# Kernel tuning notes

Measured on AMD Instinct MI355X. Metric: run time of the kernel, lower is better.

Reference implementation:

```python
import jax, jax.numpy as jnp
import numpy as np
import math

H, DH, DP, DE = 8, 16, 128, 32   # heads, dim_head, dim_p_embd, dim_embd
M = 64                            # number of random features
EPS = 1e-4                        # softmax_kernel eps
LN_EPS = 1e-5


def gelu(x):
    # exact tanh-approx gelu used in the source
    return 0.5 * x * (1.0 + jnp.tanh(math.sqrt(2.0 / math.pi) * (x + 0.044715 * x ** 3)))


def layernorm(x, w, b):
    mu = x.mean(-1, keepdims=True)
    var = ((x - mu) ** 2).mean(-1, keepdims=True)
    return (x - mu) / jnp.sqrt(var + LN_EPS) * w + b


def softmax_kernel(data, proj, is_query):
    # FAVOR+ positive random-feature softmax kernel
    dn = data.shape[-1] ** -0.25
    ratio = proj.shape[0] ** -0.5
    dash = jnp.einsum('bhnd,md->bhnm', dn * data, proj)
    diag = (data ** 2).sum(-1, keepdims=True) * (0.5 * dn * dn)
    unnorm = ratio * jnp.exp(dash - diag)
    if is_query:
        mx = jax.lax.stop_gradient(jnp.max(dash, axis=-1, keepdims=True))
    else:
        mx = jax.lax.stop_gradient(jnp.max(dash, axis=(-1, -2), keepdims=True))
    return unnorm * jnp.exp(-mx) + ratio * EPS, unnorm


def linear_attention(q, k, v):
    k_sum = k.sum(-2)                                        # (b,h,m)
    d_inv = 1.0 / jnp.einsum('bhnm,bhm->bhn', q, k_sum)
    ctx = jnp.einsum('bhnm,bhne->bhme', k, v)                # (b,h,m,d)
    return jnp.einsum('bhme,bhnm,bhn->bhne', ctx, q, d_inv)


def heads(t):
    b, n, _ = t.shape
    return t.reshape(b, n, H, DH).transpose(0, 2, 1, 3)      # b n (h d) -> b h n d


def setup_inputs() -> dict:
    key = jax.random.key(0)
    ks = jax.random.split(key, 12)
    B, NCTX, NQ = 16, 3200, 3072
    std = 0.02
    return {
        'x': jax.random.normal(ks[0], (B, NCTX, DE), jnp.float32),
        'y': jax.random.normal(ks[1], (2, B, NQ, DP), jnp.float32),
        'proj': jax.random.normal(ks[2], (M, DH), jnp.float32),
        'ln1_w': jnp.ones((DP,), jnp.float32), 'ln1_b': jnp.zeros((DP,), jnp.float32),
        'ln2_w': jnp.ones((DE,), jnp.float32), 'ln2_b': jnp.zeros((DE,), jnp.float32),
        'ln4_w': jnp.ones((DP,), jnp.float32), 'ln4_b': jnp.zeros((DP,), jnp.float32),
        'fc_w': std * jax.random.normal(ks[3], (DP, DP), jnp.float32),
        'fc_b': jnp.zeros((DP,), jnp.float32),
        'pr_w': std * jax.random.normal(ks[4], (DP, DP), jnp.float32),
        'pr_b': jnp.zeros((DP,), jnp.float32),
        'wq': std * jax.random.normal(ks[5], (DP, DP), jnp.float32),
        'wk': std * jax.random.normal(ks[6], (DP, DE), jnp.float32),
        'wv': std * jax.random.normal(ks[7], (DP, DE), jnp.float32),
        'wo': std * jax.random.normal(ks[8], (DP, DP), jnp.float32),
        'wo_b': jnp.zeros((DP,), jnp.float32),
    }


def reference(x, y, proj, ln1_w, ln1_b, ln2_w, ln2_b, ln4_w, ln4_b,
              fc_w, fc_b, pr_w, pr_b, wq, wk, wv, wo, wo_b):
    # --- MLP(dim_p_embd) pre-attention residual (Conv1D: x @ W + b) ---
    h = gelu(layernorm(y, ln4_w, ln4_b) @ fc_w + fc_b)
    y1 = h @ pr_w + pr_b + y                                 # (2,B,NQ,DP)

    xq = layernorm(y1, ln1_w, ln1_b)
    ctx = layernorm(x, ln2_w, ln2_b)
    B, NCTX, _ = x.shape
    NQ = y.shape[2]

    q = heads(xq.reshape(-1, NQ, DP) @ wq.T)                 # (2B,H,NQ,DH)
    k = heads(ctx @ wk.T)                                    # (B,H,NCTX,DH)
    v = heads(ctx @ wv.T)

    # temporal split: doubles the batch, drops first/last s tokens
    s = NCTX * 2 // 50
    k2 = jnp.concatenate([k[None, :, :, :-s], k[None, :, :, s:]], 0).reshape(2 * B, H, NCTX - s, DH)
    v2 = jnp.concatenate([v[None, :, :, :-s], v[None, :, :, s:]], 0).reshape(2 * B, H, NCTX - s, DH)

    qf, q_unnorm = softmax_kernel(q, proj, True)
    kf, k_unnorm = softmax_kernel(k2, proj, False)
    out = linear_attention(qf, kf, v2)                       # (2B,H,NQ,DH)

    out = out.transpose(0, 2, 1, 3).reshape(2 * B, NQ, DP) @ wo.T + wo_b
    y_out = y1 + out.reshape(y.shape)
    return y_out, q_unnorm[:, :, None], k_unnorm[:, :, None]
```

## Files before the change

### kernel.cpp

```cpp
#include <hip/hip_runtime.h>
#include <math.h>

constexpr int cH = 8;
constexpr int cDP = 128;
constexpr int cM = 64;
constexpr int cB = 16;
constexpr int cNCTX = 3200;
constexpr int cNQ = 3072;
constexpr int cSHIFT = 128;
constexpr int ROWS_Q = 2 * cB * cNQ;
constexpr int ROWS_KV = cB * cNCTX;
constexpr float cRATIO = 0.125f;
constexpr float cEPST = 0.125e-4f;
constexpr float cLNEPS = 1e-5f;

typedef float f32x4 __attribute__((ext_vector_type(4)));
typedef short short8 __attribute__((ext_vector_type(8)));
typedef _Float16 half2 __attribute__((ext_vector_type(2)));

#define MFMA16x16(a, b, c) __builtin_amdgcn_mfma_f32_16x16x32_bf16((a), (b), (c), 0, 0, 0)

__device__ __forceinline__ float wmax64(float v) {
#pragma unroll
  for (int o = 32; o; o >>= 1) v = fmaxf(v, __shfl_xor(v, o));
  return v;
}
__device__ __forceinline__ float wsum64(float v) {
#pragma unroll
  for (int o = 32; o; o >>= 1) v += __shfl_xor(v, o);
  return v;
}
__device__ __forceinline__ float gelu_f(float x) {
  return 0.5f * x * (1.0f + tanhf(0.79788456080286536f * (x + 0.044715f * x * x * x)));
}
__device__ __forceinline__ unsigned int bf16r(float f) {
  unsigned int x = __float_as_uint(f);
  return (x + 0x7fffu + ((x >> 16) & 1u)) >> 16;
}
__device__ __forceinline__ unsigned int f16r(float f) {
  _Float16 hh = (_Float16)f;
  unsigned short u;
  __builtin_memcpy(&u, &hh, 2);
  return (unsigned int)u;
}
__device__ __forceinline__ int swz(int row, int k) {
  return row * 128 + ((((k >> 3) ^ (row & 15)) << 3) | (k & 7));
}

__global__ __launch_bounds__(256) void k0_prep(
    const float* __restrict__ fcw, const float* __restrict__ prw,
    const float* __restrict__ wq, const float* __restrict__ wo,
    unsigned short* __restrict__ fcT, unsigned short* __restrict__ prT,
    unsigned short* __restrict__ wqT, unsigned short* __restrict__ woT) {
  const int mat = blockIdx.x;
  const float* src = mat == 0 ? fcw : mat == 1 ? prw : mat == 2 ? wq : wo;
  unsigned short* dst = mat == 0 ? fcT : mat == 1 ? prT : mat == 2 ? wqT : woT;
  const bool tr = (mat < 2);
  for (int i = threadIdx.x; i < 16384; i += 256) {
    int n = i >> 7, k = i & 127;
    float f = tr ? src[k * 128 + n] : src[i];
    dst[swz(n, k)] = (unsigned short)(mat == 2 ? f16r(f) : bf16r(f));
  }
}

__global__ __launch_bounds__(256, 2) void k1_mlp(
    const float* __restrict__ y,
    const float* __restrict__ ln4w, const float* __restrict__ ln4b,
    const unsigned short* __restrict__ fcT, const float* __restrict__ fcb,
    const unsigned short* __restrict__ prT, const float* __restrict__ prb,
    float* __restrict__ y1) {
  __shared__ unsigned short wfc[16384];
  __shared__ unsigned short wpr[16384];
  __shared__ unsigned short xb[4096];
  __shared__ unsigned short hb[4096];
  const int tid = threadIdx.x;
  {
    const uint4* s1 = (const uint4*)fcT; uint4* d1 = (uint4*)wfc;
    const uint4* s2 = (const uint4*)prT; uint4* d2 = (uint4*)wpr;
    for (int i = tid; i < 2048; i += 256) { d1[i] = s1[i]; d2[i] = s2[i]; }
  }
  const int lane = tid & 63, wv = tid >> 6;
  const int lrow = tid >> 3, lsub = tid & 7;
  const int colbase = wv * 32;
  float fb[2], pb[2];
#pragma unroll
  for (int ct = 0; ct < 2; ++ct) {
    int col = colbase + ct * 16 + (lane & 15);
    fb[ct] = fcb[col];
    pb[ct] = prb[col];
  }
  float lw[16], lb[16];
  *(float4*)&lw[0] = *(const float4*)(ln4w + lsub * 16 + 0);
  *(float4*)&lw[4] = *(const float4*)(ln4w + lsub * 16 + 4);
  *(float4*)&lw[8] = *(const float4*)(ln4w + lsub * 16 + 8);
  *(float4*)&lw[12] = *(const float4*)(ln4w + lsub * 16 + 12);
  *(float4*)&lb[0] = *(const float4*)(ln4b + lsub * 16 + 0);
  *(float4*)&lb[4] = *(const float4*)(ln4b + lsub * 16 + 4);
  *(float4*)&lb[8] = *(const float4*)(ln4b + lsub * 16 + 8);
  *(float4*)&lb[12] = *(const float4*)(ln4b + lsub * 16 + 12);
  uint4* xb4 = (uint4*)xb;
  __syncthreads();

  for (int g = blockIdx.x; g < ROWS_Q / 32; g += gridDim.x) {
    const int r0 = g * 32;
    {
      const float* yr = y + (size_t)(r0 + lrow) * 128 + lsub * 16;
      float v[16];
      *(float4*)&v[0] = *(const float4*)(yr + 0);
      *(float4*)&v[4] = *(const float4*)(yr + 4);
      *(float4*)&v[8] = *(const float4*)(yr + 8);
      *(float4*)&v[12] = *(const float4*)(yr + 12);
      float s = 0.f, q = 0.f;
#pragma unroll
      for (int j = 0; j < 16; ++j) { s += v[j]; q += v[j] * v[j]; }
#pragma unroll
      for (int o = 1; o <= 4; o <<= 1) { s += __shfl_xor(s, o); q += __shfl_xor(q, o); }
      float mu = s * (1.0f / 128.0f);
      float rs = rsqrtf(q * (1.0f / 128.0f) - mu * mu + cLNEPS);
      unsigned int us[8];
#pragma unroll
      for (int j = 0; j < 8; ++j) {
        float f0 = (v[2 * j] - mu) * rs * lw[2 * j] + lb[2 * j];
        float f1 = (v[2 * j + 1] - mu) * rs * lw[2 * j + 1] + lb[2 * j + 1];
        us[j] = bf16r(f0) | (bf16r(f1) << 16);
      }
      int s0 = (lsub * 2) ^ (lrow & 15), s1 = (lsub * 2 + 1) ^ (lrow & 15);
      xb4[lrow * 16 + s0] = make_uint4(us[0], us[1], us[2], us[3]);
      xb4[lrow * 16 + s1] = make_uint4(us[4], us[5], us[6], us[7]);
    }
    __syncthreads();
    {
      f32x4 acc[2][2] = {{{0.f,0.f,0.f,0.f},{0.f,0.f,0.f,0.f}},
                         {{0.f,0.f,0.f,0.f},{0.f,0.f,0.f,0.f}}};
#pragma unroll
      for (int kc = 0; kc < 4; ++kc) {
        short8 af[2], bfv[2];
#pragma unroll
        for (int rt = 0; rt < 2; ++rt) {
          int row = rt * 16 + (lane & 15);
          int slot = ((lane >> 4) + kc * 4) ^ (row & 15);
          af[rt] = *(const short8*)&xb[row * 128 + slot * 8];
        }
#pragma unroll
        for (int ct = 0; ct < 2; ++ct) {
          int col = colbase + ct * 16 + (lane & 15);
          int slot = ((lane >> 4) + kc * 4) ^ (col & 15);
          bfv[ct] = *(const short8*)&wfc[col * 128 + slot * 8];
        }
#pragma unroll
        for (int rt = 0; rt < 2; ++rt)
#pragma unroll
          for (int ct = 0; ct < 2; ++ct)
            acc[rt][ct] = MFMA16x16(af[rt], bfv[ct], acc[rt][ct]);
      }
#pragma unroll
      for (int rt = 0; rt < 2; ++rt)
#pragma unroll
        for (int ct = 0; ct < 2; ++ct) {
          int col = colbase + ct * 16 + (lane & 15);
#pragma unroll
          for (int reg = 0; reg < 4; ++reg) {
            int row = rt * 16 + (lane >> 4) * 4 + reg;
            hb[swz(row, col)] = (unsigned short)bf16r(gelu_f(acc[rt][ct][reg] + fb[ct]));
          }
        }
    }
    __syncthreads();
    {
      f32x4 a2[2][2] = {{{0.f,0.f,0.f,0.f},{0.f,0.f,0.f,0.f}},
                        {{0.f,0.f,0.f,0.f},{0.f,0.f,0.f,0.f}}};
#pragma unroll
      for (int kc = 0; kc < 4; ++kc) {
        short8 af[2], bfv[2];
#pragma unroll
        for (int rt = 0; rt < 2; ++rt) {
          int row = rt * 16 + (lane & 15);
          int slot = ((lane >> 4) + kc * 4) ^ (row & 15);
          af[rt] = *(const short8*)&hb[row * 128 + slot * 8];
        }
#pragma unroll
        for (int ct = 0; ct < 2; ++ct) {
          int col = colbase + ct * 16 + (lane & 15);
          int slot = ((lane >> 4) + kc * 4) ^ (col & 15);
          bfv[ct] = *(const short8*)&wpr[col * 128 + slot * 8];
        }
#pragma unroll
        for (int rt = 0; rt < 2; ++rt)
#pragma unroll
          for (int ct = 0; ct < 2; ++ct)
            a2[rt][ct] = MFMA16x16(af[rt], bfv[ct], a2[rt][ct]);
      }
#pragma unroll
      for (int rt = 0; rt < 2; ++rt)
#pragma unroll
        for (int ct = 0; ct < 2; ++ct) {
          int col = colbase + ct * 16 + (lane & 15);
#pragma unroll
          for (int reg = 0; reg < 4; ++reg) {
            int row = rt * 16 + (lane >> 4) * 4 + reg;
            size_t o = (size_t)(r0 + row) * 128 + col;
            y1[o] = a2[rt][ct][reg] + pb[ct] + y[o];
          }
        }
    }
    __syncthreads();
  }
}

__global__ __launch_bounds__(512) void k2_kv(
    const float* __restrict__ x,
    const float* __restrict__ ln2w, const float* __restrict__ ln2b,
    const float* __restrict__ wkw, const float* __restrict__ wvw,
    float* __restrict__ kbuf, float* __restrict__ vbuf) {
  __shared__ float wkT[32 * cDP];
  __shared__ float wvT[32 * cDP];
  __shared__ float xbs[16][32];
  const int tid = threadIdx.x;
  for (int i = tid; i < 32 * cDP; i += 512) {
    int j = i >> 5, d = i & 31;
    wkT[d * cDP + j] = wkw[i];
    wvT[d * cDP + j] = wvw[i];
  }
  const int dl = tid & 31, rl = tid >> 5;
  const int col = tid & 127, rh = tid >> 7;
  const float l2w = ln2w[dl], l2b = ln2b[dl];
  __syncthreads();
  for (int g = blockIdx.x; g < ROWS_KV / 16; g += gridDim.x) {
    const int r0 = g * 16;
    __syncthreads();
    {
      float v = x[(size_t)(r0 + rl) * 32 + dl];
      float s = v, q = v * v;
#pragma unroll
      for (int o = 16; o; o >>= 1) { s += __shfl_xor(s, o); q += __shfl_xor(q, o); }
      float mu = s * (1.0f / 32.0f);
      float var = q * (1.0f / 32.0f) - mu * mu;
      xbs[rl][dl] = (v - mu) * rsqrtf(var + cLNEPS) * l2w + l2b;
    }
    __syncthreads();
    float ak0 = 0, ak1 = 0, ak2 = 0, ak3 = 0, av0 = 0, av1 = 0, av2 = 0, av3 = 0;
    for (int d = 0; d < 32; d += 4) {
      float4 v0 = *(const float4*)&xbs[rh * 4 + 0][d];
      float4 v1 = *(const float4*)&xbs[rh * 4 + 1][d];
      float4 v2 = *(const float4*)&xbs[rh * 4 + 2][d];
      float4 v3 = *(const float4*)&xbs[rh * 4 + 3][d];
      float k0 = wkT[(d + 0) * cDP + col], k1 = wkT[(d + 1) * cDP + col];
      float k2 = wkT[(d + 2) * cDP + col], k3 = wkT[(d + 3) * cDP + col];
      float u0 = wvT[(d + 0) * cDP + col], u1 = wvT[(d + 1) * cDP + col];
      float u2 = wvT[(d + 2) * cDP + col], u3 = wvT[(d + 3) * cDP + col];
      ak0 += v0.x * k0 + v0.y * k1 + v0.z * k2 + v0.w * k3;
      ak1 += v1.x * k0 + v1.y * k1 + v1.z * k2 + v1.w * k3;
      ak2 += v2.x * k0 + v2.y * k1 + v2.z * k2 + v2.w * k3;
      ak3 += v3.x * k0 + v3.y * k1 + v3.z * k2 + v3.w * k3;
      av0 += v0.x * u0 + v0.y * u1 + v0.z * u2 + v0.w * u3;
      av1 += v1.x * u0 + v1.y * u1 + v1.z * u2 + v1.w * u3;
      av2 += v2.x * u0 + v2.y * u1 + v2.z * u2 + v2.w * u3;
      av3 += v3.x * u0 + v3.y * u1 + v3.z * u2 + v3.w * u3;
    }
    kbuf[(size_t)(r0 + rh * 4 + 0) * cDP + col] = ak0;
    kbuf[(size_t)(r0 + rh * 4 + 1) * cDP + col] = ak1;
    kbuf[(size_t)(r0 + rh * 4 + 2) * cDP + col] = ak2;
    kbuf[(size_t)(r0 + rh * 4 + 3) * cDP + col] = ak3;
    vbuf[(size_t)(r0 + rh * 4 + 0) * cDP + col] = av0;
    vbuf[(size_t)(r0 + rh * 4 + 1) * cDP + col] = av1;
    vbuf[(size_t)(r0 + rh * 4 + 2) * cDP + col] = av2;
    vbuf[(size_t)(r0 + rh * 4 + 3) * cDP + col] = av3;
  }
}

__global__ __launch_bounds__(512) void k4_kun(
    const float* __restrict__ kbuf, const float* __restrict__ proj,
    float* __restrict__ k_un, float* __restrict__ tmax) {
  __shared__ float kb[16][cDP];
  const int tid = threadIdx.x;
  const int m = tid & 63, h = tid >> 6, lane = tid & 63;
  float pr[16];
#pragma unroll
  for (int d = 0; d < 16; ++d) pr[d] = proj[m * 16 + d];
  for (int g = blockIdx.x; g < ROWS_KV / 16; g += gridDim.x) {
    const int r0 = g * 16;
    __syncthreads();
    for (int i = tid; i < 16 * cDP; i += 512)
      kb[i >> 7][i & 127] = kbuf[(size_t)(r0 + (i >> 7)) * cDP + (i & 127)];
    __syncthreads();
    const int b = r0 / cNCTX;
    for (int r4 = 0; r4 < 16; r4 += 4) {
      float dashv[4];
#pragma unroll
      for (int j = 0; j < 4; ++j) {
        int r = r4 + j;
        float4 q0 = *(const float4*)&kb[r][h * 16 + 0];
        float4 q1 = *(const float4*)&kb[r][h * 16 + 4];
        float4 q2 = *(const float4*)&kb[r][h * 16 + 8];
        float4 q3 = *(const float4*)&kb[r][h * 16 + 12];
        float dash = q0.x * pr[0] + q0.y * pr[1] + q0.z * pr[2] + q0.w * pr[3]
                   + q1.x * pr[4] + q1.y * pr[5] + q1.z * pr[6] + q1.w * pr[7]
                   + q2.x * pr[8] + q2.y * pr[9] + q2.z * pr[10] + q2.w * pr[11]
                   + q3.x * pr[12] + q3.y * pr[13] + q3.z * pr[14] + q3.w * pr[15];
        dash *= 0.5f;
        float ss = q0.x * q0.x + q0.y * q0.y + q0.z * q0.z + q0.w * q0.w
                 + q1.x * q1.x + q1.y * q1.y + q1.z * q1.z + q1.w * q1.w
                 + q2.x * q2.x + q2.y * q2.y + q2.z * q2.z + q2.w * q2.w
                 + q3.x * q3.x + q3.y * q3.y + q3.z * q3.z + q3.w * q3.w;
        dashv[j] = dash;
        float un = cRATIO * __expf(dash - 0.125f * ss);
        int t = r0 + r - b * cNCTX;
        if (t < cNQ)
          k_un[((size_t)(b * cH + h) * cNQ + t) * cM + m] = un;
        if (t >= cSHIFT)
          k_un[((size_t)((b + cB) * cH + h) * cNQ + (t - cSHIFT)) * cM + m] = un;
      }
      float m0 = dashv[0], m1 = dashv[1], m2 = dashv[2], m3 = dashv[3];
#pragma unroll
      for (int o = 32; o; o >>= 1) {
        float t0 = __shfl_xor(m0, o), t1 = __shfl_xor(m1, o);
        float t2 = __shfl_xor(m2, o), t3 = __shfl_xor(m3, o);
        m0 = fmaxf(m0, t0); m1 = fmaxf(m1, t1);
        m2 = fmaxf(m2, t2); m3 = fmaxf(m3, t3);
      }
      if (lane == 0) {
        int tb = (b * cH + h) * cNCTX + (r0 - b * cNCTX) + r4;
        tmax[tb + 0] = m0;
        tmax[tb + 1] = m1;
        tmax[tb + 2] = m2;
        tmax[tb + 3] = m3;
      }
    }
  }
}

__global__ __launch_bounds__(256) void k4b_mxk(
    const float* __restrict__ tmax, float* __restrict__ mxk) {
  const int bh = blockIdx.x;
  const int tid = threadIdx.x;
  float m0 = -1e30f, m1 = -1e30f;
  for (int t = tid; t < cNCTX; t += 256) {
    float v = tmax[bh * cNCTX + t];
    if (t < cNQ) m0 = fmaxf(m0, v);
    if (t >= cSHIFT) m1 = fmaxf(m1, v);
  }
  __shared__ float s0[256], s1[256];
  s0[tid] = m0; s1[tid] = m1;
  __syncthreads();
  for (int s = 128; s; s >>= 1) {
    if (tid < s) { s0[tid] = fmaxf(s0[tid], s0[tid + s]); s1[tid] = fmaxf(s1[tid], s1[tid + s]); }
    __syncthreads();
  }
  if (tid == 0) { mxk[bh] = s0[0]; mxk[bh + 128] = s1[0]; }
}

__global__ __launch_bounds__(256) void k5a_ctx(
    const float* __restrict__ k_un, const float* __restrict__ vbuf,
    const float* __restrict__ mxk,
    float* __restrict__ part_c, float* __restrict__ part_k) {
  const int bbh = blockIdx.x;
  const int ch = blockIdx.y;
  const int bb = bbh >> 3, h = bbh & 7;
  const int b = bb & 15, toff = (bb >> 4) * cSHIFT;
  const float ek = expf(-mxk[bbh]);
  const int tid = threadIdx.x, m = tid & 63, eq = tid >> 6;
  __shared__ float ub[64][64];
  __shared__ float vb[64][16];
  float c0 = 0, c1 = 0, c2 = 0, c3 = 0, ks = 0;
  const int nb = ch * 512;
  for (int n0 = nb; n0 < nb + 512; n0 += 64) {
    for (int i = tid; i < 64 * 64; i += 256)
      ub[i >> 6][i & 63] = k_un[((size_t)bbh * cNQ + n0 + (i >> 6)) * cM + (i & 63)];
    for (int i = tid; i < 64 * 16; i += 256)
      vb[i >> 4][i & 15] = vbuf[((size_t)(b * cNCTX) + toff + n0 + (i >> 4)) * cDP + h * 16 + (i & 15)];
    __syncthreads();
#pragma unroll 4
    for (int nn = 0; nn < 64; ++nn) {
      float kf = ub[nn][m] * ek + cEPST;
      ks += kf;
      float4 vv = *(const float4*)&vb[nn][eq * 4];
      c0 += kf * vv.x; c1 += kf * vv.y; c2 += kf * vv.z; c3 += kf * vv.w;
    }
    __syncthreads();
  }
  size_t po = (size_t)ch * 256 + bbh;
  part_c[po * 1024 + m * 16 + eq * 4 + 0] = c0;
  part_c[po * 1024 + m * 16 + eq * 4 + 1] = c1;
  part_c[po * 1024 + m * 16 + eq * 4 + 2] = c2;
  part_c[po * 1024 + m * 16 + eq * 4 + 3] = c3;
  if (eq == 0) part_k[po * 64 + m] = ks;
}

__global__ __launch_bounds__(256) void k5a2_red(
    const float* __restrict__ part_c, const float* __restrict__ part_k,
    float* __restrict__ ctx2, float* __restrict__ ksum) {
  const int bbh = blockIdx.x;
  const int tid = threadIdx.x;
  for (int i = tid; i < 1024; i += 256) {
    float s = 0;
#pragma unroll
    for (int ch = 0; ch < 6; ++ch) s += part_c[((size_t)ch * 256 + bbh) * 1024 + i];
    ctx2[bbh * 1024 + i] = s;
  }
  if (tid < 64) {
    float s = 0;
#pragma unroll
    for (int ch = 0; ch < 6; ++ch) s += part_k[((size_t)ch * 256 + bbh) * 64 + tid];
    ksum[bbh * cM + tid] = s;
  }
}

__global__ __launch_bounds__(512, 4) void kq_fused2(
    const float* __restrict__ y1,
    const float* __restrict__ ln1w, const float* __restrict__ ln1b,
    const unsigned short* __restrict__ wqT, const float* __restrict__ proj,
    const float* __restrict__ ctx2, const float* __restrict__ ksum,
    float* __restrict__ q_un, float* __restrict__ attn) {
  __shared__ unsigned short wqs[128 * 128];
  __shared__ unsigned short xb[32 * 128];
  __shared__ float qb[32][132];
  __shared__ unsigned short qfl[8][16][72];
  __shared__ float dvv[8][16];
  const int tid = threadIdx.x;
  const int bb = blockIdx.y;
  {
    const uint4* s1 = (const uint4*)wqT; uint4* d1 = (uint4*)wqs;
    for (int i = tid; i < 2048; i += 512) d1[i] = s1[i];
  }
  const int lane = tid & 63, wvid = tid >> 6;
  const int lrow = tid >> 4, c8 = tid & 15;
  const int cx = tid & 31, ry2 = tid >> 5;
  const int m = lane;
  const int h = wvid;
  float pr[16];
#pragma unroll
  for (int d = 0; d < 16; ++d) pr[d] = proj[m * 16 + d];
  short8 bfr[2], bks[2];
  {
    const float* cp = ctx2 + (size_t)(bb * cH + h) * 1024;
    const float* kp = ksum + (size_t)(bb * cH + h) * cM;
#pragma unroll
    for (int kh = 0; kh < 2; ++kh) {
      short8 bfv, bkv;
#pragma unroll
      for (int j = 0; j < 8; ++j) {
        int mm = kh * 32 + (lane >> 4) * 8 + j;
        ((unsigned short*)&bfv)[j] = (unsigned short)bf16r(cp[mm * 16 + (lane & 15)]);
        ((unsigned short*)&bkv)[j] =
            ((lane & 15) == 0) ? (unsigned short)bf16r(kp[mm]) : (unsigned short)0;
      }
      bfr[kh] = bfv;
      bks[kh] = bkv;
    }
  }
  float lw[8], lb[8];
  *(float4*)&lw[0] = *(const float4*)(ln1w + c8 * 8 + 0);
  *(float4*)&lw[4] = *(const float4*)(ln1w + c8 * 8 + 4);
  *(float4*)&lb[0] = *(const float4*)(ln1b + c8 * 8 + 0);
  *(float4*)&lb[4] = *(const float4*)(ln1b + c8 * 8 + 4);
  uint4* xb4 = (uint4*)xb;
  const uint4* wq4 = (const uint4*)wqs;
  __syncthreads();

  for (int tile = blockIdx.x; tile < 96; tile += 16) {
    const int n0 = tile * 32;
    const size_t r0g = (size_t)bb * cNQ + n0;
    {
      const float* yr = y1 + (r0g + lrow) * 128 + c8 * 8;
      float v[8];
      *(float4*)&v[0] = *(const float4*)(yr + 0);
      *(float4*)&v[4] = *(const float4*)(yr + 4);
      float s = 0.f, q = 0.f;
#pragma unroll
      for (int j = 0; j < 8; ++j) { s += v[j]; q += v[j] * v[j]; }
#pragma unroll
      for (int o = 1; o <= 8; o <<= 1) { s += __shfl_xor(s, o); q += __shfl_xor(q, o); }
      float mu = s * (1.0f / 128.0f);
      float rs = rsqrtf(q * (1.0f / 128.0f) - mu * mu + cLNEPS);
      unsigned int us[4];
#pragma unroll
      for (int j = 0; j < 4; ++j) {
        float f0 = (v[2 * j] - mu) * rs * lw[2 * j] + lb[2 * j];
        float f1 = (v[2 * j + 1] - mu) * rs * lw[2 * j + 1] + lb[2 * j + 1];
        us[j] = f16r(f0) | (f16r(f1) << 16);
      }
      xb4[lrow * 16 + (c8 ^ (lrow & 15))] = make_uint4(us[0], us[1], us[2], us[3]);
    }
    __syncthreads();
    {
      float acc[2][4] = {};
#pragma unroll 2
      for (int kg = 0; kg < 16; ++kg) {
        uint4 xv[2], wv[4];
#pragma unroll
        for (int rr = 0; rr < 2; ++rr) {
          int r = ry2 * 2 + rr;
          xv[rr] = xb4[r * 16 + (kg ^ (r & 15))];
        }
#pragma unroll
        for (int cc = 0; cc < 4; ++cc) {
          int c = cx + 32 * cc;
          wv[cc] = wq4[c * 16 + (kg ^ (c & 15))];
        }
#pragma unroll
        for (int cc = 0; cc < 4; ++cc) {
          const half2* wh = (const half2*)&wv[cc];
#pragma unroll
          for (int rr = 0; rr < 2; ++rr) {
            const half2* xh = (const half2*)&xv[rr];
#pragma unroll
            for (int p = 0; p < 4; ++p)
              acc[rr][cc] = __builtin_amdgcn_fdot2(xh[p], wh[p], acc[rr][cc], false);
          }
        }
      }
#pragma unroll
      for (int rr = 0; rr < 2; ++rr)
#pragma unroll
        for (int cc = 0; cc < 4; ++cc)
          qb[ry2 * 2 + rr][cx + 32 * cc] = acc[rr][cc];
    }
    __syncthreads();
    float ssv;
    {
      int r = lane & 31;
      float4 s0 = *(const float4*)&qb[r][h * 16 + 0];
      float4 s1 = *(const float4*)&qb[r][h * 16 + 4];
      float4 s2 = *(const float4*)&qb[r][h * 16 + 8];
      float4 s3 = *(const float4*)&qb[r][h * 16 + 12];
      ssv = s0.x * s0.x + s0.y * s0.y + s0.z * s0.z + s0.w * s0.w
          + s1.x * s1.x + s1.y * s1.y + s1.z * s1.z + s1.w * s1.w
          + s2.x * s2.x + s2.y * s2.y + s2.z * s2.z + s2.w * s2.w
          + s3.x * s3.x + s3.y * s3.y + s3.z * s3.z + s3.w * s3.w;
    }
#pragma unroll
    for (int half = 0; half < 2; ++half) {
      for (int rr = 0; rr < 16; rr += 4) {
        float dashv[4], unv[4];
#pragma unroll
        for (int j = 0; j < 4; ++j) {
          int r = half * 16 + rr + j;
          float4 a0 = *(const float4*)&qb[r][h * 16 + 0];
          float4 a1 = *(const float4*)&qb[r][h * 16 + 4];
          float4 a2 = *(const float4*)&qb[r][h * 16 + 8];
          float4 a3 = *(const float4*)&qb[r][h * 16 + 12];
          float dash = a0.x * pr[0] + a0.y * pr[1] + a0.z * pr[2] + a0.w * pr[3]
                     + a1.x * pr[4] + a1.y * pr[5] + a1.z * pr[6] + a1.w * pr[7]
                     + a2.x * pr[8] + a2.y * pr[9] + a2.z * pr[10] + a2.w * pr[11]
                     + a3.x * pr[12] + a3.y * pr[13] + a3.z * pr[14] + a3.w * pr[15];
          dash *= 0.5f;
          dashv[j] = dash;
          float ss = __shfl(ssv, r);
          unv[j] = cRATIO * __expf(dash - 0.125f * ss);
          q_un[((size_t)(bb * cH + h) * cNQ + n0 + r) * cM + m] = unv[j];
        }
        float m0 = dashv[0], m1 = dashv[1], m2 = dashv[2], m3 = dashv[3];
#pragma unroll
        for (int o = 32; o; o >>= 1) {
          float t0 = __shfl_xor(m0, o), t1 = __shfl_xor(m1, o);
          float t2 = __shfl_xor(m2, o), t3 = __shfl_xor(m3, o);
          m0 = fmaxf(m0, t0); m1 = fmaxf(m1, t1);
          m2 = fmaxf(m2, t2); m3 = fmaxf(m3, t3);
        }
        qfl[wvid][rr + 0][lane] = (unsigned short)bf16r(unv[0] * __expf(-m0) + cEPST);
        qfl[wvid][rr + 1][lane] = (unsigned short)bf16r(unv[1] * __expf(-m1) + cEPST);
        qfl[wvid][rr + 2][lane] = (unsigned short)bf16r(unv[2] * __expf(-m2) + cEPST);
        qfl[wvid][rr + 3][lane] = (unsigned short)bf16r(unv[3] * __expf(-m3) + cEPST);
      }
      {
        const unsigned short* qp = &qfl[wvid][0][0];
        int ab = (lane & 15) * 72 + (lane >> 4) * 8;
        short8 a0 = *(const short8*)&qp[ab];
        short8 a1 = *(const short8*)&qp[ab + 32];
        f32x4 cd = {0.f, 0.f, 0.f, 0.f};
        cd = MFMA16x16(a0, bks[0], cd);
        cd = MFMA16x16(a1, bks[1], cd);
        if ((lane & 15) == 0) {
#pragma unroll
          for (int reg = 0; reg < 4; ++reg)
            dvv[wvid][(lane >> 4) * 4 + reg] = 1.0f / cd[reg];
        }
        f32x4 c = {0.f, 0.f, 0.f, 0.f};
        c = MFMA16x16(a0, bfr[0], c);
        c = MFMA16x16(a1, bfr[1], c);
#pragma unroll
        for (int reg = 0; reg < 4; ++reg) {
          int rloc = (lane >> 4) * 4 + reg;
          attn[(r0g + half * 16 + rloc) * cDP + h * 16 + (lane & 15)] =
              c[reg] * dvv[wvid][rloc];
        }
      }
    }
    __syncthreads();
  }
}

__global__ __launch_bounds__(256, 2) void k6_wo(
    const float* __restrict__ attn,
    const unsigned short* __restrict__ woT, const float* __restrict__ wob,
    const float* __restrict__ y1, float* __restrict__ yout) {
  __shared__ unsigned short wos[16384];
  __shared__ unsigned short xb[4096];
  const int tid = threadIdx.x;
  {
    const uint4* s1 = (const uint4*)woT; uint4* d1 = (uint4*)wos;
    for (int i = tid; i < 2048; i += 256) d1[i] = s1[i];
  }
  const int lane = tid & 63, wv = tid >> 6;
  const int lrow = tid >> 3, lsub = tid & 7;
  const int colbase = wv * 32;
  float wb[2];
#pragma unroll
  for (int ct = 0; ct < 2; ++ct) wb[ct] = wob[colbase + ct * 16 + (lane & 15)];
  uint4* xb4 = (uint4*)xb;
  __syncthreads();
  for (int g = blockIdx.x; g < ROWS_Q / 32; g += gridDim.x) {
    const int r0 = g * 32;
    {
      const float* ar = attn + (size_t)(r0 + lrow) * 128 + lsub * 16;
      float v[16];
      *(float4*)&v[0] = *(const float4*)(ar + 0);
      *(float4*)&v[4] = *(const float4*)(ar + 4);
      *(float4*)&v[8] = *(const float4*)(ar + 8);
      *(float4*)&v[12] = *(const float4*)(ar + 12);
      unsigned int us[8];
#pragma unroll
      for (int j = 0; j < 8; ++j)
        us[j] = bf16r(v[2 * j]) | (bf16r(v[2 * j + 1]) << 16);
      int s0 = (lsub * 2) ^ (lrow & 15), s1 = (lsub * 2 + 1) ^ (lrow & 15);
      xb4[lrow * 16 + s0] = make_uint4(us[0], us[1], us[2], us[3]);
      xb4[lrow * 16 + s1] = make_uint4(us[4], us[5], us[6], us[7]);
    }
    __syncthreads();
    {
      f32x4 acc[2][2] = {{{0.f,0.f,0.f,0.f},{0.f,0.f,0.f,0.f}},
                         {{0.f,0.f,0.f,0.f},{0.f,0.f,0.f,0.f}}};
#pragma unroll
      for (int kc = 0; kc < 4; ++kc) {
        short8 af[2], bfv[2];
#pragma unroll
        for (int rt = 0; rt < 2; ++rt) {
          int row = rt * 16 + (lane & 15);
          int slot = ((lane >> 4) + kc * 4) ^ (row & 15);
          af[rt] = *(const short8*)&xb[row * 128 + slot * 8];
        }
#pragma unroll
        for (int ct = 0; ct < 2; ++ct) {
          int col = colbase + ct * 16 + (lane & 15);
          int slot = ((lane >> 4) + kc * 4) ^ (col & 15);
          bfv[ct] = *(const short8*)&wos[col * 128 + slot * 8];
        }
#pragma unroll
        for (int rt = 0; rt < 2; ++rt)
#pragma unroll
          for (int ct = 0; ct < 2; ++ct)
            acc[rt][ct] = MFMA16x16(af[rt], bfv[ct], acc[rt][ct]);
      }
#pragma unroll
      for (int rt = 0; rt < 2; ++rt)
#pragma unroll
        for (int ct = 0; ct < 2; ++ct) {
          int col = colbase + ct * 16 + (lane & 15);
#pragma unroll
          for (int reg = 0; reg < 4; ++reg) {
            int row = rt * 16 + (lane >> 4) * 4 + reg;
            size_t o = (size_t)(r0 + row) * 128 + col;
            yout[o] = acc[rt][ct][reg] + wb[ct] + y1[o];
          }
        }
    }
    __syncthreads();
  }
}

extern "C" void kernel_launch(void* const* d_in, const int* in_sizes, int n_in,
                              void* d_out, int out_size, void* d_ws, size_t ws_size,
                              hipStream_t stream) {
  (void)in_sizes; (void)n_in; (void)out_size; (void)ws_size;
  const float* x = (const float*)d_in[0];
  const float* y = (const float*)d_in[1];
  const float* proj = (const float*)d_in[2];
  const float* ln1w = (const float*)d_in[3];
  const float* ln1b = (const float*)d_in[4];
  const float* ln2w = (const float*)d_in[5];
  const float* ln2b = (const float*)d_in[6];
  const float* ln4w = (const float*)d_in[7];
  const float* ln4b = (const float*)d_in[8];
  const float* fcw = (const float*)d_in[9];
  const float* fcb = (const float*)d_in[10];
  const float* prw = (const float*)d_in[11];
  const float* prb = (const float*)d_in[12];
  const float* wq = (const float*)d_in[13];
  const float* wk = (const float*)d_in[14];
  const float* wv = (const float*)d_in[15];
  const float* wo = (const float*)d_in[16];
  const float* wob = (const float*)d_in[17];

  float* out = (float*)d_out;
  float* q_un = out + 12582912;
  float* k_un = out + 62914560;

  float* ws = (float*)d_ws;
  float* y1 = ws;
  float* kbuf = ws + 12582912;
  float* vbuf = ws + 19136512;
  float* part_c = ws + 12582912;
  float* part_k = ws + 14155776;
  float* attn = ws + 12582912;
  float* tmax = ws + 26476544;
  float* mxk = ws + 26886144;
  float* ksum = ws + 26886400;
  float* ctx2 = ws + 26902784;
  unsigned short* fcT = (unsigned short*)(ws + 27164928);
  unsigned short* prT = fcT + 16384;
  unsigned short* wqT = prT + 16384;
  unsigned short* woT = wqT + 16384;

  k0_prep<<<dim3(4), dim3(256), 0, stream>>>(fcw, prw, wq, wo, fcT, prT, wqT, woT);
  k1_mlp<<<dim3(512), dim3(256), 0, stream>>>(y, ln4w, ln4b, fcT, fcb, prT, prb, y1);
  k2_kv<<<dim3(400), dim3(512), 0, stream>>>(x, ln2w, ln2b, wk, wv, kbuf, vbuf);
  k4_kun<<<dim3(400), dim3(512), 0, stream>>>(kbuf, proj, k_un, tmax);
  k4b_mxk<<<dim3(128), dim3(256), 0, stream>>>(tmax, mxk);
  k5a_ctx<<<dim3(256, 6), dim3(256), 0, stream>>>(k_un, vbuf, mxk, part_c, part_k);
  k5a2_red<<<dim3(256), dim3(256), 0, stream>>>(part_c, part_k, ctx2, ksum);
  kq_fused2<<<dim3(16, 32), dim3(512), 0, stream>>>(y1, ln1w, ln1b, wqT, proj,
                                                    ctx2, ksum, q_un, attn);
  k6_wo<<<dim3(512), dim3(256), 0, stream>>>(attn, woT, wob, y1, out);
}
```

Before: 398.7 us.

## Fuse key-context accumulation into k_un kernel via atomics and algebraic rescale

The k-feature kernel now also accumulates the unscaled context (k_un^T v) and key sums per block in registers, then atomically adds them into zeroed global buffers. The per-(batch,head) max scale and eps term are applied afterwards in a small kernel, using the identity ctx = ek*raw + eps*sum(v). This removes the separate pass that re-read the large k_un array and the partial-sum reduction kernel. It adds float atomics, which make the summation order nondeterministic, and extra register pressure in k4.

```diff
diff --git a/kernel.cpp b/kernel.cpp
--- a/kernel.cpp
+++ b/kernel.cpp
@@ -25,11 +25,6 @@
   for (int o = 32; o; o >>= 1) v = fmaxf(v, __shfl_xor(v, o));
   return v;
 }
-__device__ __forceinline__ float wsum64(float v) {
-#pragma unroll
-  for (int o = 32; o; o >>= 1) v += __shfl_xor(v, o);
-  return v;
-}
 __device__ __forceinline__ float gelu_f(float x) {
   return 0.5f * x * (1.0f + tanhf(0.79788456080286536f * (x + 0.044715f * x * x * x)));
 }
@@ -46,13 +41,27 @@
 __device__ __forceinline__ int swz(int row, int k) {
   return row * 128 + ((((k >> 3) ^ (row & 15)) << 3) | (k & 7));
 }
+__device__ __forceinline__ void fma16(float4 (&a)[4], float s,
+                                      const float4& w0, const float4& w1,
+                                      const float4& w2, const float4& w3) {
+  a[0].x += s * w0.x; a[0].y += s * w0.y; a[0].z += s * w0.z; a[0].w += s * w0.w;
+  a[1].x += s * w1.x; a[1].y += s * w1.y; a[1].z += s * w1.z; a[1].w += s * w1.w;
+  a[2].x += s * w2.x; a[2].y += s * w2.y; a[2].z += s * w2.z; a[2].w += s * w2.w;
+  a[3].x += s * w3.x; a[3].y += s * w3.y; a[3].z += s * w3.z; a[3].w += s * w3.w;
+}
 
 __global__ __launch_bounds__(256) void k0_prep(
     const float* __restrict__ fcw, const float* __restrict__ prw,
     const float* __restrict__ wq, const float* __restrict__ wo,
     unsigned short* __restrict__ fcT, unsigned short* __restrict__ prT,
-    unsigned short* __restrict__ wqT, unsigned short* __restrict__ woT) {
+    unsigned short* __restrict__ wqT, unsigned short* __restrict__ woT,
+    float* __restrict__ ctx_raw) {
   const int mat = blockIdx.x;
+  if (mat >= 4) {
+    for (int i = (mat - 4) * 256 + threadIdx.x; i < 278528; i += 8 * 256)
+      ctx_raw[i] = 0.f;
+    return;
+  }
   const float* src = mat == 0 ? fcw : mat == 1 ? prw : mat == 2 ? wq : wo;
   unsigned short* dst = mat == 0 ? fcT : mat == 1 ? prT : mat == 2 ? wqT : woT;
   const bool tr = (mat < 2);
@@ -269,21 +278,30 @@
 }
 
 __global__ __launch_bounds__(512) void k4_kun(
-    const float* __restrict__ kbuf, const float* __restrict__ proj,
-    float* __restrict__ k_un, float* __restrict__ tmax) {
+    const float* __restrict__ kbuf, const float* __restrict__ vbuf,
+    const float* __restrict__ proj,
+    float* __restrict__ k_un, float* __restrict__ tmax,
+    float* __restrict__ ctx_raw, float* __restrict__ ks_raw) {
   __shared__ float kb[16][cDP];
+  __shared__ float vb[16][cDP];
   const int tid = threadIdx.x;
   const int m = tid & 63, h = tid >> 6, lane = tid & 63;
   float pr[16];
 #pragma unroll
   for (int d = 0; d < 16; ++d) pr[d] = proj[m * 16 + d];
-  for (int g = blockIdx.x; g < ROWS_KV / 16; g += gridDim.x) {
+  const int b = blockIdx.x / 25, c = blockIdx.x % 25;
+  float4 ca0[4] = {{0,0,0,0},{0,0,0,0},{0,0,0,0},{0,0,0,0}};
+  float4 ca1[4] = {{0,0,0,0},{0,0,0,0},{0,0,0,0},{0,0,0,0}};
+  float ks0 = 0.f, ks1 = 0.f;
+  for (int i = 0; i < 8; ++i) {
+    const int g = b * 200 + c + 25 * i;
     const int r0 = g * 16;
     __syncthreads();
-    for (int i = tid; i < 16 * cDP; i += 512)
-      kb[i >> 7][i & 127] = kbuf[(size_t)(r0 + (i >> 7)) * cDP + (i & 127)];
-    __syncthreads();
-    const int b = r0 / cNCTX;
+    for (int j = tid; j < 16 * cDP; j += 512) {
+      kb[j >> 7][j & 127] = kbuf[(size_t)(r0 + (j >> 7)) * cDP + (j & 127)];
+      vb[j >> 7][j & 127] = vbuf[(size_t)(r0 + (j >> 7)) * cDP + (j & 127)];
+    }
+    __syncthreads();
     for (int r4 = 0; r4 < 16; r4 += 4) {
       float dashv[4];
 #pragma unroll
@@ -305,10 +323,20 @@
         dashv[j] = dash;
         float un = cRATIO * __expf(dash - 0.125f * ss);
         int t = r0 + r - b * cNCTX;
-        if (t < cNQ)
+        float4 w0 = *(const float4*)&vb[r][h * 16 + 0];
+        float4 w1 = *(const float4*)&vb[r][h * 16 + 4];
+        float4 w2 = *(const float4*)&vb[r][h * 16 + 8];
+        float4 w3 = *(const float4*)&vb[r][h * 16 + 12];
+        if (t < cNQ) {
           k_un[((size_t)(b * cH + h) * cNQ + t) * cM + m] = un;
-        if (t >= cSHIFT)
+          ks0 += un;
+          fma16(ca0, un, w0, w1, w2, w3);
+        }
+        if (t >= cSHIFT) {
           k_un[((size_t)((b + cB) * cH + h) * cNQ + (t - cSHIFT)) * cM + m] = un;
+          ks1 += un;
+          fma16(ca1, un, w0, w1, w2, w3);
+        }
       }
       float m0 = dashv[0], m1 = dashv[1], m2 = dashv[2], m3 = dashv[3];
 #pragma unroll
@@ -326,6 +354,23 @@
         tmax[tb + 3] = m3;
       }
     }
+  }
+  {
+    float* c0p = ctx_raw + (size_t)(b * cH + h) * 1024 + m * 16;
+    float* c1p = ctx_raw + (size_t)((b + cB) * cH + h) * 1024 + m * 16;
+#pragma unroll
+    for (int q4 = 0; q4 < 4; ++q4) {
+      atomicAdd(&c0p[q4 * 4 + 0], ca0[q4].x);
+      atomicAdd(&c0p[q4 * 4 + 1], ca0[q4].y);
+      atomicAdd(&c0p[q4 * 4 + 2], ca0[q4].z);
+      atomicAdd(&c0p[q4 * 4 + 3], ca0[q4].w);
+      atomicAdd(&c1p[q4 * 4 + 0], ca1[q4].x);
+      atomicAdd(&c1p[q4 * 4 + 1], ca1[q4].y);
+      atomicAdd(&c1p[q4 * 4 + 2], ca1[q4].z);
+      atomicAdd(&c1p[q4 * 4 + 3], ca1[q4].w);
+    }
+    atomicAdd(&ks_raw[(b * cH + h) * cM + m], ks0);
+    atomicAdd(&ks_raw[((b + cB) * cH + h) * cM + m], ks1);
   }
 }
 
@@ -349,60 +394,37 @@
   if (tid == 0) { mxk[bh] = s0[0]; mxk[bh + 128] = s1[0]; }
 }
 
-__global__ __launch_bounds__(256) void k5a_ctx(
-    const float* __restrict__ k_un, const float* __restrict__ vbuf,
-    const float* __restrict__ mxk,
-    float* __restrict__ part_c, float* __restrict__ part_k) {
+__global__ __launch_bounds__(256) void k5s_scale(
+    const float* __restrict__ ctx_raw, const float* __restrict__ ks_raw,
+    const float* __restrict__ vbuf, const float* __restrict__ mxk,
+    float* __restrict__ ctx2, float* __restrict__ ksum) {
   const int bbh = blockIdx.x;
-  const int ch = blockIdx.y;
   const int bb = bbh >> 3, h = bbh & 7;
   const int b = bb & 15, toff = (bb >> 4) * cSHIFT;
   const float ek = expf(-mxk[bbh]);
-  const int tid = threadIdx.x, m = tid & 63, eq = tid >> 6;
-  __shared__ float ub[64][64];
-  __shared__ float vb[64][16];
-  float c0 = 0, c1 = 0, c2 = 0, c3 = 0, ks = 0;
-  const int nb = ch * 512;
-  for (int n0 = nb; n0 < nb + 512; n0 += 64) {
-    for (int i = tid; i < 64 * 64; i += 256)
-      ub[i >> 6][i & 63] = k_un[((size_t)bbh * cNQ + n0 + (i >> 6)) * cM + (i & 63)];
-    for (int i = tid; i < 64 * 16; i += 256)
-      vb[i >> 4][i & 15] = vbuf[((size_t)(b * cNCTX) + toff + n0 + (i >> 4)) * cDP + h * 16 + (i & 15)];
-    __syncthreads();
-#pragma unroll 4
-    for (int nn = 0; nn < 64; ++nn) {
-      float kf = ub[nn][m] * ek + cEPST;
-      ks += kf;
-      float4 vv = *(const float4*)&vb[nn][eq * 4];
-      c0 += kf * vv.x; c1 += kf * vv.y; c2 += kf * vv.z; c3 += kf * vv.w;
-    }
-    __syncthreads();
-  }
-  size_t po = (size_t)ch * 256 + bbh;
-  part_c[po * 1024 + m * 16 + eq * 4 + 0] = c0;
-  part_c[po * 1024 + m * 16 + eq * 4 + 1] = c1;
-  part_c[po * 1024 + m * 16 + eq * 4 + 2] = c2;
-  part_c[po * 1024 + m * 16 + eq * 4 + 3] = c3;
-  if (eq == 0) part_k[po * 64 + m] = ks;
-}
-
-__global__ __launch_bounds__(256) void k5a2_red(
-    const float* __restrict__ part_c, const float* __restrict__ part_k,
-    float* __restrict__ ctx2, float* __restrict__ ksum) {
-  const int bbh = blockIdx.x;
   const int tid = threadIdx.x;
-  for (int i = tid; i < 1024; i += 256) {
-    float s = 0;
-#pragma unroll
-    for (int ch = 0; ch < 6; ++ch) s += part_c[((size_t)ch * 256 + bbh) * 1024 + i];
-    ctx2[bbh * 1024 + i] = s;
-  }
-  if (tid < 64) {
-    float s = 0;
-#pragma unroll
-    for (int ch = 0; ch < 6; ++ch) s += part_k[((size_t)ch * 256 + bbh) * 64 + tid];
-    ksum[bbh * cM + tid] = s;
-  }
+  __shared__ float vsp[16][16];
+  __shared__ float vse[16];
+  {
+    const int e = tid & 15, gr = tid >> 4;
+    float a = 0.f;
+    for (int t = gr; t < cNQ; t += 16)
+      a += vbuf[((size_t)(b * cNCTX) + toff + t) * cDP + h * 16 + e];
+    vsp[gr][e] = a;
+  }
+  __syncthreads();
+  if (tid < 16) {
+    float a = 0.f;
+#pragma unroll
+    for (int gr = 0; gr < 16; ++gr) a += vsp[gr][tid];
+    vse[tid] = a;
+  }
+  __syncthreads();
+  for (int i = tid; i < 1024; i += 256)
+    ctx2[(size_t)bbh * 1024 + i] =
+        ek * ctx_raw[(size_t)bbh * 1024 + i] + cEPST * vse[i & 15];
+  if (tid < 64)
+    ksum[bbh * cM + tid] = ek * ks_raw[bbh * cM + tid] + 3072.0f * cEPST;
 }
 
 __global__ __launch_bounds__(512, 4) void kq_fused2(
@@ -699,9 +721,9 @@
   float* y1 = ws;
   float* kbuf = ws + 12582912;
   float* vbuf = ws + 19136512;
-  float* part_c = ws + 12582912;
-  float* part_k = ws + 14155776;
   float* attn = ws + 12582912;
+  float* ctx_raw = ws + 25690112;
+  float* ks_raw = ws + 25952256;
   float* tmax = ws + 26476544;
   float* mxk = ws + 26886144;
   float* ksum = ws + 26886400;
@@ -711,13 +733,12 @@
   unsigned short* wqT = prT + 16384;
   unsigned short* woT = wqT + 16384;
 
-  k0_prep<<<dim3(4), dim3(256), 0, stream>>>(fcw, prw, wq, wo, fcT, prT, wqT, woT);
+  k0_prep<<<dim3(12), dim3(256), 0, stream>>>(fcw, prw, wq, wo, fcT, prT, wqT, woT, ctx_raw);
   k1_mlp<<<dim3(512), dim3(256), 0, stream>>>(y, ln4w, ln4b, fcT, fcb, prT, prb, y1);
   k2_kv<<<dim3(400), dim3(512), 0, stream>>>(x, ln2w, ln2b, wk, wv, kbuf, vbuf);
-  k4_kun<<<dim3(400), dim3(512), 0, stream>>>(kbuf, proj, k_un, tmax);
+  k4_kun<<<dim3(400), dim3(512), 0, stream>>>(kbuf, vbuf, proj, k_un, tmax, ctx_raw, ks_raw);
   k4b_mxk<<<dim3(128), dim3(256), 0, stream>>>(tmax, mxk);
-  k5a_ctx<<<dim3(256, 6), dim3(256), 0, stream>>>(k_un, vbuf, mxk, part_c, part_k);
-  k5a2_red<<<dim3(256), dim3(256), 0, stream>>>(part_c, part_k, ctx2, ksum);
+  k5s_scale<<<dim3(256), dim3(256), 0, stream>>>(ctx_raw, ks_raw, vbuf, mxk, ctx2, ksum);
   kq_fused2<<<dim3(16, 32), dim3(512), 0, stream>>>(y1, ln1w, ln1b, wqT, proj,
                                                     ctx2, ksum, q_un, attn);
   k6_wo<<<dim3(512), dim3(256), 0, stream>>>(attn, woT, wob, y1, out);
```

After: 709.6 us. 1.78x slower.
